# Performance work log

Hardware: AMD Instinct MI355X
Metric: run time of the kernel (lower is better)

The kernel has to match this reference:

```python
import jax, jax.numpy as jnp
import numpy as np

L, NFEAT, J, S = 100000, 256, 128, 8  # nodes, features, hidden, samples_per_k


def setup_inputs() -> dict:
    key = jax.random.key(0)
    ks = jax.random.split(key, 8)
    X = jax.random.normal(ks[0], (L, NFEAT), dtype=jnp.float32)
    # sampled 2-permutation neighbor indices (first and second element of each permutation)
    idx0 = jax.random.randint(ks[1], (S, L), 0, L)
    idx1 = jax.random.randint(ks[2], (S, L), 0, L)
    def lin(k, fan_in, fan_out):
        bound = 1.0 / np.sqrt(fan_in)
        kw, kb = jax.random.split(k)
        W = jax.random.uniform(kw, (fan_in, fan_out), jnp.float32, -bound, bound)
        b = jax.random.uniform(kb, (fan_out,), jnp.float32, -bound, bound)
        return W, b
    W_h1, b_h1 = lin(ks[3], NFEAT, J)      # h1: Linear(nfeat, J)
    W_g1, b_g1 = lin(ks[4], 2 * J, J)      # g1: Linear(2J, J)
    W_f, b_f = lin(ks[5], J, 2)            # final1: Linear(J, 2)
    return {"X": X, "W_h1": W_h1, "b_h1": b_h1, "W_g1": W_g1, "b_g1": b_g1,
            "W_f": W_f, "b_f": b_f, "idx0": idx0, "idx1": idx1}


def reference(X, W_h1, b_h1, W_g1, b_g1, W_f, b_f, idx0, idx1):
    # h(x) = relu(h1(x)); since h is only ever applied to rows of X, compute once and gather.
    H = jax.nn.relu(X @ W_h1 + b_h1)                     # (L, J)
    # fk(k=2): mean over samples of g(cat(h(X[perm0]), h(X[perm1])))
    pair = jnp.concatenate([H[idx0], H[idx1]], axis=-1)  # (S, L, 2J) irregular gather
    E = jnp.mean(jax.nn.relu(pair @ W_g1 + b_g1), axis=0)  # (L, J)
    E = jax.nn.relu(E)                                   # relu of mean of relus (faithful)
    # E = g(cat(h(X), E))
    E = jax.nn.relu(jnp.concatenate([H, E], axis=-1) @ W_g1 + b_g1)  # (L, J)
    # yhat = final1(E)
    return E @ W_f + b_f                                 # (L, 2)
```

## Files before the change

kernel.cpp:

```cpp
#include <hip/hip_runtime.h>

#define L_NODES 100000
#define NFEAT   256
#define JDIM    128

typedef __bf16 bf16x8 __attribute__((ext_vector_type(8)));
typedef __bf16 bf16x4 __attribute__((ext_vector_type(4)));
typedef float  floatx4 __attribute__((ext_vector_type(4)));

__global__ __launch_bounds__(256) void k_prep(
    const float* __restrict__ Wh, const float* __restrict__ Wg,
    __bf16* __restrict__ WtH, __bf16* __restrict__ WtG2)
{
    int i = blockIdx.x * 256 + threadIdx.x;
    int n = i >> 8, k = i & 255;
    WtH[i] = (__bf16)Wh[k * JDIM + n];
    int n2 = i >> 7, k2 = i & 127;
    WtG2[i] = (n2 < 128) ? (__bf16)Wg[k2 * JDIM + n2]
                         : (__bf16)Wg[(128 + k2) * JDIM + (n2 - 128)];
}

__global__ __launch_bounds__(256) void k_h1uv(
    const float* __restrict__ X, const __bf16* __restrict__ WtH,
    const __bf16* __restrict__ WtG2, const float* __restrict__ b,
    __bf16* __restrict__ U, __bf16* __restrict__ V)
{
    __shared__ __bf16 As[64 * 264];
    __shared__ __bf16 Hs[64 * 136];

    const int tid  = threadIdx.x;
    const int row0 = blockIdx.x * 64;
    const int wave = tid >> 6, lane = tid & 63;
    const int lm = lane & 15, lq = lane >> 4;

    bf16x8 b1[2][8];
    #pragma unroll
    for (int nt = 0; nt < 2; ++nt) {
        int ntg = wave * 2 + nt;
        #pragma unroll
        for (int ks = 0; ks < 8; ++ks)
            b1[nt][ks] = *(const bf16x8*)(WtH + (size_t)(ntg * 16 + lm) * 256 + ks * 32 + lq * 8);
    }

    #pragma unroll
    for (int it = 0; it < 16; ++it) {
        int f4  = it * 256 + tid;
        int row = f4 >> 6, c4 = f4 & 63;
        int grow = row0 + row; if (grow >= L_NODES) grow = L_NODES - 1;
        float4 v = *(const float4*)(X + (size_t)grow * NFEAT + c4 * 4);
        bf16x4 o; o[0]=(__bf16)v.x; o[1]=(__bf16)v.y; o[2]=(__bf16)v.z; o[3]=(__bf16)v.w;
        *(bf16x4*)&As[row * 264 + c4 * 4] = o;
    }
    __syncthreads();

    floatx4 acc1[4][2] = {};
    #pragma unroll
    for (int ks = 0; ks < 8; ++ks) {
        bf16x8 af[4];
        #pragma unroll
        for (int t = 0; t < 4; ++t)
            af[t] = *(const bf16x8*)&As[(t * 16 + lm) * 264 + ks * 32 + lq * 8];
        #pragma unroll
        for (int t = 0; t < 4; ++t)
            #pragma unroll
            for (int nt = 0; nt < 2; ++nt)
                acc1[t][nt] = __builtin_amdgcn_mfma_f32_16x16x32_bf16(
                    af[t], b1[nt][ks], acc1[t][nt], 0, 0, 0);
    }

    bf16x8 b2[4][4];
    #pragma unroll
    for (int nt = 0; nt < 4; ++nt) {
        int ntg = wave * 4 + nt;
        #pragma unroll
        for (int ks = 0; ks < 4; ++ks)
            b2[nt][ks] = *(const bf16x8*)(WtG2 + (size_t)(ntg * 16 + lm) * 128 + ks * 32 + lq * 8);
    }

    #pragma unroll
    for (int nt = 0; nt < 2; ++nt) {
        int col = (wave * 2 + nt) * 16 + lm;
        float bias = b[col];
        #pragma unroll
        for (int t = 0; t < 4; ++t)
            #pragma unroll
            for (int p = 0; p < 4; ++p)
                Hs[(t * 16 + lq * 4 + p) * 136 + col] =
                    (__bf16)fmaxf(acc1[t][nt][p] + bias, 0.f);
    }
    __syncthreads();

    floatx4 acc2[4][4] = {};
    #pragma unroll
    for (int ks = 0; ks < 4; ++ks) {
        bf16x8 af[4];
        #pragma unroll
        for (int t = 0; t < 4; ++t)
            af[t] = *(const bf16x8*)&Hs[(t * 16 + lm) * 136 + ks * 32 + lq * 8];
        #pragma unroll
        for (int t = 0; t < 4; ++t)
            #pragma unroll
            for (int nt = 0; nt < 4; ++nt)
                acc2[t][nt] = __builtin_amdgcn_mfma_f32_16x16x32_bf16(
                    af[t], b2[nt][ks], acc2[t][nt], 0, 0, 0);
    }

    #pragma unroll
    for (int nt = 0; nt < 4; ++nt) {
        int col = (wave * 4 + nt) * 16 + lm;
        #pragma unroll
        for (int t = 0; t < 4; ++t)
            #pragma unroll
            for (int p = 0; p < 4; ++p)
                As[(t * 16 + lq * 4 + p) * 264 + col] = (__bf16)acc2[t][nt][p];
    }
    __syncthreads();

    #pragma unroll
    for (int it = 0; it < 8; ++it) {
        int fid = it * 256 + tid;
        int row = fid >> 5, c8 = fid & 31;
        int grow = row0 + row;
        if (grow < L_NODES) {
            int col = c8 * 8;
            bf16x8 v = *(bf16x8*)&As[row * 264 + col];
            if (col < 128) *(bf16x8*)(U + (size_t)grow * JDIM + col) = v;
            else           *(bf16x8*)(V + (size_t)grow * JDIM + (col - 128)) = v;
        }
    }
}

__global__ __launch_bounds__(256) void k_gather(
    const __bf16* __restrict__ U, const __bf16* __restrict__ V,
    const float* __restrict__ b,
    const int* __restrict__ idx0, const int* __restrict__ idx1,
    __bf16* __restrict__ E1b)
{
    __shared__ int s0[8][16], s1[8][16];

    const int tid = threadIdx.x;
    const int i0  = blockIdx.x * 16;

    if (tid < 128) {
        int s = tid >> 4, il = tid & 15;
        s0[s][il] = idx0[(size_t)s * L_NODES + i0 + il];
    } else {
        int t = tid - 128, s = t >> 4, il = t & 15;
        s1[s][il] = idx1[(size_t)s * L_NODES + i0 + il];
    }
    __syncthreads();

    const int il = tid >> 4;
    const int c0 = (tid & 15) * 8;

    float bias[8];
    *(float4*)&bias[0] = *(const float4*)(b + c0);
    *(float4*)&bias[4] = *(const float4*)(b + c0 + 4);

    float acc[8] = {};
    #pragma unroll
    for (int s = 0; s < 8; ++s) {
        int r0 = s0[s][il], r1 = s1[s][il];
        bf16x8 u = *(const bf16x8*)(U + (size_t)r0 * JDIM + c0);
        bf16x8 v = *(const bf16x8*)(V + (size_t)r1 * JDIM + c0);
        #pragma unroll
        for (int p = 0; p < 8; ++p)
            acc[p] += fmaxf((float)u[p] + (float)v[p] + bias[p], 0.f);
    }

    bf16x8 o;
    #pragma unroll
    for (int p = 0; p < 8; ++p)
        o[p] = (__bf16)fmaxf(acc[p] * 0.125f, 0.f);
    *(bf16x8*)(E1b + (size_t)(i0 + il) * JDIM + c0) = o;
}

__global__ __launch_bounds__(256) void k_final2(
    const __bf16* __restrict__ U, const __bf16* __restrict__ E1b,
    const __bf16* __restrict__ WtGv, const float* __restrict__ bg,
    const float* __restrict__ Wf, const float* __restrict__ bf,
    float* __restrict__ out)
{
    __shared__ __bf16 E1s[64 * 136];
    __shared__ __bf16 Us [64 * 136];
    __shared__ float  part[4][64][2];

    const int tid  = threadIdx.x;
    const int row0 = blockIdx.x * 64;
    const int wave = tid >> 6, lane = tid & 63;
    const int lm = lane & 15, lq = lane >> 4;

    bf16x8 b3[2][4];
    #pragma unroll
    for (int nt = 0; nt < 2; ++nt) {
        int ntg = wave * 2 + nt;
        #pragma unroll
        for (int ks = 0; ks < 4; ++ks)
            b3[nt][ks] = *(const bf16x8*)(WtGv + (size_t)(ntg * 16 + lm) * 128 + ks * 32 + lq * 8);
    }

    #pragma unroll
    for (int it = 0; it < 8; ++it) {
        int fid = it * 256 + tid;
        int half = fid >> 10;
        int r = (fid & 1023) >> 4, c8 = fid & 15;
        int grow = row0 + r; if (grow >= L_NODES) grow = L_NODES - 1;
        const __bf16* src = half ? (U + (size_t)grow * JDIM + c8 * 8)
                                 : (E1b + (size_t)grow * JDIM + c8 * 8);
        __bf16* dst = half ? &Us[r * 136 + c8 * 8] : &E1s[r * 136 + c8 * 8];
        *(bf16x8*)dst = *(const bf16x8*)src;
    }
    __syncthreads();

    floatx4 acc[4][2] = {};
    #pragma unroll
    for (int ks = 0; ks < 4; ++ks) {
        bf16x8 af[4];
        #pragma unroll
        for (int t = 0; t < 4; ++t)
            af[t] = *(const bf16x8*)&E1s[(t * 16 + lm) * 136 + ks * 32 + lq * 8];
        #pragma unroll
        for (int t = 0; t < 4; ++t)
            #pragma unroll
            for (int nt = 0; nt < 2; ++nt)
                acc[t][nt] = __builtin_amdgcn_mfma_f32_16x16x32_bf16(
                    af[t], b3[nt][ks], acc[t][nt], 0, 0, 0);
    }

    float bias[2], wf0[2], wf1[2];
    #pragma unroll
    for (int nt = 0; nt < 2; ++nt) {
        int col = (wave * 2 + nt) * 16 + lm;
        bias[nt] = bg[col];
        wf0[nt] = Wf[col * 2 + 0];
        wf1[nt] = Wf[col * 2 + 1];
    }
    #pragma unroll
    for (int t = 0; t < 4; ++t) {
        float p0[4], p1[4];
        #pragma unroll
        for (int p = 0; p < 4; ++p) {
            int r = t * 16 + lq * 4 + p;
            float a0 = 0.f, a1 = 0.f;
            #pragma unroll
            for (int nt = 0; nt < 2; ++nt) {
                int col = (wave * 2 + nt) * 16 + lm;
                float e2 = fmaxf((float)Us[r * 136 + col] + acc[t][nt][p] + bias[nt], 0.f);
                a0 = fmaf(e2, wf0[nt], a0);
                a1 = fmaf(e2, wf1[nt], a1);
            }
            p0[p] = a0; p1[p] = a1;
        }
        #pragma unroll
        for (int m = 1; m <= 8; m <<= 1)
            #pragma unroll
            for (int p = 0; p < 4; ++p) {
                p0[p] += __shfl_xor(p0[p], m, 16);
                p1[p] += __shfl_xor(p1[p], m, 16);
            }
        if (lm == 0)
            #pragma unroll
            for (int p = 0; p < 4; ++p) {
                part[wave][t * 16 + lq * 4 + p][0] = p0[p];
                part[wave][t * 16 + lq * 4 + p][1] = p1[p];
            }
    }
    __syncthreads();

    if (tid < 128) {
        int row = tid >> 1, o = tid & 1;
        int grow = row0 + row;
        if (grow < L_NODES)
            out[(size_t)grow * 2 + o] =
                part[0][row][o] + part[1][row][o] + part[2][row][o] + part[3][row][o] + bf[o];
    }
}

extern "C" void kernel_launch(void* const* d_in, const int* in_sizes, int n_in,
                              void* d_out, int out_size, void* d_ws, size_t ws_size,
                              hipStream_t stream) {
    const float* X    = (const float*)d_in[0];
    const float* W_h1 = (const float*)d_in[1];
    const float* b_h1 = (const float*)d_in[2];
    const float* W_g1 = (const float*)d_in[3];
    const float* b_g1 = (const float*)d_in[4];
    const float* W_f  = (const float*)d_in[5];
    const float* b_f  = (const float*)d_in[6];
    const int*   idx0 = (const int*)d_in[7];
    const int*   idx1 = (const int*)d_in[8];
    float* out = (float*)d_out;

    __bf16* E1b  = (__bf16*)d_ws;
    __bf16* U    = E1b + (size_t)L_NODES * JDIM;
    __bf16* V    = U   + (size_t)L_NODES * JDIM;
    __bf16* WtH  = V   + (size_t)L_NODES * JDIM;
    __bf16* WtG2 = WtH + 32768;
    __bf16* WtGv = WtG2 + 128 * 128;

    k_prep<<<128, 256, 0, stream>>>(W_h1, W_g1, WtH, WtG2);
    k_h1uv<<<(L_NODES + 63) / 64, 256, 0, stream>>>(X, WtH, WtG2, b_h1, U, V);
    k_gather<<<L_NODES / 16, 256, 0, stream>>>(U, V, b_g1, idx0, idx1, E1b);
    k_final2<<<(L_NODES + 63) / 64, 256, 0, stream>>>(U, E1b, WtGv, b_g1, W_f, b_f, out);
}
```

Baseline: 276.4 us.

## Fuse neighbor gather-mean into final GEMM kernel, dropping E1 intermediate

Merges the gather/mean kernel into the final matmul kernel. Each 64-row block now loads its sampled indices into shared memory, gathers U/V rows, and writes the relu-mean E1 tile straight into shared memory. This removes the global write and reread of the bf16 E1 buffer (about 25 MB each way) and one kernel launch. In exchange, each block carries more registers and shared memory, and the gather latency now sits in the same kernel as the MFMA work, which may lower occupancy.

Result: faster. 267.8 us (-3.1%).

```diff
diff --git a/kernel.cpp b/kernel.cpp
--- a/kernel.cpp
+++ b/kernel.cpp
@@ -130,57 +130,14 @@
     }
 }
 
-__global__ __launch_bounds__(256) void k_gather(
+__global__ __launch_bounds__(256) void k_gfinal(
     const __bf16* __restrict__ U, const __bf16* __restrict__ V,
-    const float* __restrict__ b,
-    const int* __restrict__ idx0, const int* __restrict__ idx1,
-    __bf16* __restrict__ E1b)
-{
-    __shared__ int s0[8][16], s1[8][16];
-
-    const int tid = threadIdx.x;
-    const int i0  = blockIdx.x * 16;
-
-    if (tid < 128) {
-        int s = tid >> 4, il = tid & 15;
-        s0[s][il] = idx0[(size_t)s * L_NODES + i0 + il];
-    } else {
-        int t = tid - 128, s = t >> 4, il = t & 15;
-        s1[s][il] = idx1[(size_t)s * L_NODES + i0 + il];
-    }
-    __syncthreads();
-
-    const int il = tid >> 4;
-    const int c0 = (tid & 15) * 8;
-
-    float bias[8];
-    *(float4*)&bias[0] = *(const float4*)(b + c0);
-    *(float4*)&bias[4] = *(const float4*)(b + c0 + 4);
-
-    float acc[8] = {};
-    #pragma unroll
-    for (int s = 0; s < 8; ++s) {
-        int r0 = s0[s][il], r1 = s1[s][il];
-        bf16x8 u = *(const bf16x8*)(U + (size_t)r0 * JDIM + c0);
-        bf16x8 v = *(const bf16x8*)(V + (size_t)r1 * JDIM + c0);
-        #pragma unroll
-        for (int p = 0; p < 8; ++p)
-            acc[p] += fmaxf((float)u[p] + (float)v[p] + bias[p], 0.f);
-    }
-
-    bf16x8 o;
-    #pragma unroll
-    for (int p = 0; p < 8; ++p)
-        o[p] = (__bf16)fmaxf(acc[p] * 0.125f, 0.f);
-    *(bf16x8*)(E1b + (size_t)(i0 + il) * JDIM + c0) = o;
-}
-
-__global__ __launch_bounds__(256) void k_final2(
-    const __bf16* __restrict__ U, const __bf16* __restrict__ E1b,
     const __bf16* __restrict__ WtGv, const float* __restrict__ bg,
     const float* __restrict__ Wf, const float* __restrict__ bf,
+    const int* __restrict__ idx0, const int* __restrict__ idx1,
     float* __restrict__ out)
 {
+    __shared__ int    sidx0[8][64], sidx1[8][64];
     __shared__ __bf16 E1s[64 * 136];
     __shared__ __bf16 Us [64 * 136];
     __shared__ float  part[4][64][2];
@@ -200,15 +157,53 @@
     }
 
     #pragma unroll
-    for (int it = 0; it < 8; ++it) {
+    for (int it = 0; it < 4; ++it) {
         int fid = it * 256 + tid;
-        int half = fid >> 10;
-        int r = (fid & 1023) >> 4, c8 = fid & 15;
-        int grow = row0 + r; if (grow >= L_NODES) grow = L_NODES - 1;
-        const __bf16* src = half ? (U + (size_t)grow * JDIM + c8 * 8)
-                                 : (E1b + (size_t)grow * JDIM + c8 * 8);
-        __bf16* dst = half ? &Us[r * 136 + c8 * 8] : &E1s[r * 136 + c8 * 8];
-        *(bf16x8*)dst = *(const bf16x8*)src;
+        int m = fid >> 9, rem = fid & 511;
+        int s = rem >> 6, il = rem & 63;
+        int gr = row0 + il; if (gr >= L_NODES) gr = L_NODES - 1;
+        int val = (m ? idx1 : idx0)[(size_t)s * L_NODES + gr];
+        if (m) sidx1[s][il] = val; else sidx0[s][il] = val;
+    }
+    #pragma unroll
+    for (int it = 0; it < 4; ++it) {
+        int fid = it * 256 + tid;
+        int r = fid >> 4, c8 = fid & 15;
+        int g = row0 + r; if (g >= L_NODES) g = L_NODES - 1;
+        *(bf16x8*)&Us[r * 136 + c8 * 8] = *(const bf16x8*)(U + (size_t)g * JDIM + c8 * 8);
+    }
+    __syncthreads();
+
+    {
+        const int c0 = (tid & 15) * 8;
+        const int rb = tid >> 4;
+        float bias[8];
+        *(float4*)&bias[0] = *(const float4*)(bg + c0);
+        *(float4*)&bias[4] = *(const float4*)(bg + c0 + 4);
+
+        float acc[4][8] = {};
+        #pragma unroll
+        for (int s = 0; s < 8; ++s) {
+            #pragma unroll
+            for (int rr = 0; rr < 4; ++rr) {
+                int r = rb + rr * 16;
+                int a0 = sidx0[s][r], a1 = sidx1[s][r];
+                bf16x8 u = *(const bf16x8*)(U + (size_t)a0 * JDIM + c0);
+                bf16x8 v = *(const bf16x8*)(V + (size_t)a1 * JDIM + c0);
+                #pragma unroll
+                for (int p = 0; p < 8; ++p)
+                    acc[rr][p] += fmaxf((float)u[p] + (float)v[p] + bias[p], 0.f);
+            }
+        }
+        #pragma unroll
+        for (int rr = 0; rr < 4; ++rr) {
+            int r = rb + rr * 16;
+            bf16x8 o;
+            #pragma unroll
+            for (int p = 0; p < 8; ++p)
+                o[p] = (__bf16)fmaxf(acc[rr][p] * 0.125f, 0.f);
+            *(bf16x8*)&E1s[r * 136 + c0] = o;
+        }
     }
     __syncthreads();
 
@@ -290,8 +285,7 @@
     const int*   idx1 = (const int*)d_in[8];
     float* out = (float*)d_out;
 
-    __bf16* E1b  = (__bf16*)d_ws;
-    __bf16* U    = E1b + (size_t)L_NODES * JDIM;
+    __bf16* U    = (__bf16*)d_ws;
     __bf16* V    = U   + (size_t)L_NODES * JDIM;
     __bf16* WtH  = V   + (size_t)L_NODES * JDIM;
     __bf16* WtG2 = WtH + 32768;
@@ -299,6 +293,6 @@
 
     k_prep<<<128, 256, 0, stream>>>(W_h1, W_g1, WtH, WtG2);
     k_h1uv<<<(L_NODES + 63) / 64, 256, 0, stream>>>(X, WtH, WtG2, b_h1, U, V);
-    k_gather<<<L_NODES / 16, 256, 0, stream>>>(U, V, b_g1, idx0, idx1, E1b);
-    k_final2<<<(L_NODES + 63) / 64, 256, 0, stream>>>(U, E1b, WtGv, b_g1, W_f, b_f, out);
-}
+    k_gfinal<<<(L_NODES + 63) / 64, 256, 0, stream>>>(U, V, WtGv, b_g1, W_f, b_f,
+                                                      idx0, idx1, out);
+}
```
